# Performance work log

Measured on AMD Instinct MI355X. Metric: run time of the kernel, lower is better.

The kernel has to match this reference:

```python
import jax, jax.numpy as jnp
import numpy as np

B, S, HID = 2, 2048, 1024
NUM_HEADS, HEAD_DIM = 16, 64
GRID_SIZE = 16                 # crop_size // patch_size
ROT_DIM = 2 * (HEAD_DIM // 3 // 2)  # = 20, per axial segment (d, h, w)


def setup_inputs() -> dict:
    key = jax.random.key(0)
    ks = jax.random.split(key, 9)
    sc = 1.0 / np.sqrt(HID)
    return {
        "hidden_states": jax.random.normal(ks[0], (B, S, HID), jnp.float32),
        "Wq": jax.random.normal(ks[1], (HID, HID), jnp.float32) * sc,
        "bq": jax.random.normal(ks[2], (HID,), jnp.float32) * 0.02,
        "Wk": jax.random.normal(ks[3], (HID, HID), jnp.float32) * sc,
        "bk": jax.random.normal(ks[4], (HID,), jnp.float32) * 0.02,
        "Wv": jax.random.normal(ks[5], (HID, HID), jnp.float32) * sc,
        "bv": jax.random.normal(ks[6], (HID,), jnp.float32) * 0.02,
        "Wo": jax.random.normal(ks[7], (HID, HID), jnp.float32) * sc,
        "bo": jax.random.normal(ks[8], (HID,), jnp.float32) * 0.02,
    }


def _rotate(x, pos):
    # x: [B, H, S, D], pos: [S] int. Matches torch rotate_queries_or_keys:
    # sin/cos are TILED (repeat) along the last dim, not interleaved.
    D = x.shape[-1]
    half = D // 2
    omega = 1.0 / (10000.0 ** (jnp.arange(half, dtype=x.dtype) / half))
    freq = pos.astype(x.dtype)[:, None] * omega           # [S, half]
    sin = jnp.tile(jnp.sin(freq), (1, 2))                 # [S, D]
    cos = jnp.tile(jnp.cos(freq), (1, 2))
    y = x.reshape(x.shape[:-1] + (half, 2))
    rot = jnp.stack((-y[..., 1], y[..., 0]), axis=-1).reshape(x.shape)
    return x * cos + rot * sin


def _apply_axial_rope(qk, frame_ids, height_ids, width_ids):
    d = ROT_DIM
    parts = [
        _rotate(qk[..., 0:d], frame_ids),
        _rotate(qk[..., d:2 * d], height_ids),
        _rotate(qk[..., 2 * d:3 * d], width_ids),
    ]
    if 3 * d < qk.shape[-1]:
        parts.append(qk[..., 3 * d:])  # un-rotated tail
    return jnp.concatenate(parts, axis=-1)


def reference(hidden_states, Wq, bq, Wk, bk, Wv, bv, Wo, bo):
    Bq, Sq, _ = hidden_states.shape

    def heads(x):  # [B,S,HID] -> [B,H,S,Dh]
        return x.reshape(Bq, Sq, NUM_HEADS, HEAD_DIM).transpose(0, 2, 1, 3)

    q = heads(hidden_states @ Wq + bq)
    k = heads(hidden_states @ Wk + bk)
    v = heads(hidden_states @ Wv + bv)

    # 3D axial position ids from flat token index
    ids = jnp.arange(Sq)
    tokens_per_frame = GRID_SIZE * GRID_SIZE
    frame_ids = ids // tokens_per_frame
    rem = ids - tokens_per_frame * frame_ids
    height_ids = rem // GRID_SIZE
    width_ids = rem - GRID_SIZE * height_ids

    k = _apply_axial_rope(k, frame_ids, height_ids, width_ids)
    q = _apply_axial_rope(q, frame_ids, height_ids, width_ids)

    scaling = HEAD_DIM ** -0.5
    scores = jnp.einsum("bhqd,bhkd->bhqk", q, k) * scaling
    probs = jax.nn.softmax(scores.astype(jnp.float32), axis=-1).astype(q.dtype)
    ctx = jnp.einsum("bhqk,bhkd->bhqd", probs, v)
    ctx = ctx.transpose(0, 2, 1, 3).reshape(Bq, Sq, HID)
    return ctx @ Wo + bo
```

## Files before the change

kernel.cpp:

```cpp
#include <hip/hip_runtime.h>
#include <hip/hip_bf16.h>

#define B_   2
#define S_   2048
#define HID_ 1024
#define NH_  16
#define HD_  64

typedef __hip_bfloat16 bf16;
typedef __attribute__((ext_vector_type(8))) short s8v;
typedef __attribute__((ext_vector_type(4))) float f4v;

#define QSCALE 0.18033688011112042f

__device__ __forceinline__ unsigned short f2b_rne(float x) {
    unsigned int u = __float_as_uint(x);
    u += 0x7fffu + ((u >> 16) & 1u);
    return (unsigned short)(u >> 16);
}

__device__ __forceinline__ void gload_lds16(const void* g, void* l) {
    __builtin_amdgcn_global_load_lds(
        (const __attribute__((address_space(1))) void*)g,
        (__attribute__((address_space(3))) void*)l, 16, 0, 0);
}

__global__ __launch_bounds__(256) void convert_x_kernel(
    const float* __restrict__ X, unsigned short* __restrict__ Xb)
{
    const int i = (blockIdx.x * 256 + threadIdx.x) * 4;
    const float4 f = *reinterpret_cast<const float4*>(X + i);
    ushort4 u;
    u.x = f2b_rne(f.x); u.y = f2b_rne(f.y); u.z = f2b_rne(f.z); u.w = f2b_rne(f.w);
    *reinterpret_cast<ushort4*>(Xb + i) = u;
}

__global__ __launch_bounds__(256) void transpose_w_kernel(
    const float* __restrict__ W0, const float* __restrict__ W1,
    const float* __restrict__ W2, const float* __restrict__ W3,
    unsigned short* __restrict__ T0, unsigned short* __restrict__ T1,
    unsigned short* __restrict__ T2, unsigned short* __restrict__ T3)
{
    const int z = blockIdx.z;
    const float* __restrict__ W = (z == 0) ? W0 : (z == 1) ? W1 : (z == 2) ? W2 : W3;
    unsigned short* __restrict__ T = (z == 0) ? T0 : (z == 1) ? T1 : (z == 2) ? T2 : T3;

    __shared__ float Tl[64][65];
    const int n0 = blockIdx.x * 64, k0 = blockIdx.y * 64;
    const int t = threadIdx.x;
    const int rr = t >> 4, c4 = (t & 15) * 4;

    #pragma unroll
    for (int i = 0; i < 4; ++i) {
        const int kr = i * 16 + rr;
        const float4 f = *reinterpret_cast<const float4*>(W + (size_t)(k0 + kr) * HID_ + n0 + c4);
        Tl[c4 + 0][kr] = f.x; Tl[c4 + 1][kr] = f.y;
        Tl[c4 + 2][kr] = f.z; Tl[c4 + 3][kr] = f.w;
    }
    __syncthreads();
    #pragma unroll
    for (int i = 0; i < 4; ++i) {
        const int nr = i * 16 + rr;
        ushort4 u;
        u.x = f2b_rne(Tl[nr][c4 + 0]); u.y = f2b_rne(Tl[nr][c4 + 1]);
        u.z = f2b_rne(Tl[nr][c4 + 2]); u.w = f2b_rne(Tl[nr][c4 + 3]);
        *reinterpret_cast<ushort4*>(T + (size_t)(n0 + nr) * HID_ + k0 + c4) = u;
    }
}

__device__ __forceinline__ void mfma_mainloop(
    const unsigned short* __restrict__ Ag, const unsigned short* __restrict__ Bg,
    unsigned short* As, unsigned short* Bs,
    int m0, int n0, int t, f4v acc[4][4])
{
    const int w = t >> 6, lane = t & 63;
    const int l15 = lane & 15, qd = lane >> 4;
    const int wm = (w & 1) * 64, wn = (w >> 1) * 64;
    const int srow = w * 8 + (lane >> 3);
    const int lc8  = (((lane & 7) ^ (lane >> 3)) * 8);

    for (int k0 = 0; k0 < HID_; k0 += 64) {
        __syncthreads();
        #pragma unroll
        for (int it = 0; it < 4; ++it) {
            const int row = it * 32 + srow;
            const int sb = (it * 256 + w * 64) * 8;
            gload_lds16(Ag + (size_t)(m0 + row) * HID_ + k0 + lc8, As + sb);
            gload_lds16(Bg + (size_t)(n0 + row) * HID_ + k0 + lc8, Bs + sb);
        }
        __syncthreads();
        #pragma unroll
        for (int kc = 0; kc < 2; ++kc) {
            const int p = ((kc * 4 + qd) ^ (l15 & 7)) * 8;
            s8v af[4], bf[4];
            #pragma unroll
            for (int mt = 0; mt < 4; ++mt)
                af[mt] = *reinterpret_cast<const s8v*>(As + (wm + mt * 16 + l15) * 64 + p);
            #pragma unroll
            for (int nt = 0; nt < 4; ++nt)
                bf[nt] = *reinterpret_cast<const s8v*>(Bs + (wn + nt * 16 + l15) * 64 + p);
            #pragma unroll
            for (int mt = 0; mt < 4; ++mt)
                #pragma unroll
                for (int nt = 0; nt < 4; ++nt)
                    acc[mt][nt] = __builtin_amdgcn_mfma_f32_16x16x32_bf16(
                        af[mt], bf[nt], acc[mt][nt], 0, 0, 0);
        }
    }
}

__global__ __launch_bounds__(256) void gemm_qkv_kernel(
    const unsigned short* __restrict__ Xb,
    const unsigned short* __restrict__ Wqt, const unsigned short* __restrict__ Wkt,
    const unsigned short* __restrict__ Wvt,
    const float* __restrict__ bq, const float* __restrict__ bk, const float* __restrict__ bv,
    unsigned short* __restrict__ Qb, unsigned short* __restrict__ Kb,
    unsigned short* __restrict__ Vt)
{
    const int z = blockIdx.z;
    const unsigned short* __restrict__ Bt = (z == 0) ? Wqt : (z == 1) ? Wkt : Wvt;
    const float* __restrict__ bias = (z == 0) ? bq : (z == 1) ? bk : bv;

    const int n0 = blockIdx.x * 128, m0 = blockIdx.y * 128;
    const int t = threadIdx.x;
    const int w = t >> 6, lane = t & 63;
    const int l15 = lane & 15, qd = lane >> 4;
    const int wm = (w & 1) * 64, wn = (w >> 1) * 64;

    __shared__ unsigned short As[128 * 64];
    __shared__ unsigned short Bs[128 * 64];

    f4v acc[4][4];
    #pragma unroll
    for (int mt = 0; mt < 4; ++mt)
        #pragma unroll
        for (int nt = 0; nt < 4; ++nt) acc[mt][nt] = (f4v){0.f, 0.f, 0.f, 0.f};

    mfma_mainloop(Xb, Bt, As, Bs, m0, n0, t, acc);

    const float osc = (z == 0) ? QSCALE : 1.f;

    #pragma unroll
    for (int nt = 0; nt < 4; ++nt) {
        const int col = n0 + wn + nt * 16 + l15;
        const int h = col >> 6, d = col & 63;
        const float bsc = bias[col];
        const int seg = d / 20;
        const int ds  = d - seg * 20;
        const float om   = __expf(-0.9210340372f * (float)(ds % 10));
        const float sign = (d & 1) ? 1.f : -1.f;

        #pragma unroll
        for (int mt = 0; mt < 4; ++mt) {
            const int mbase = m0 + wm + mt * 16 + qd * 4;
            const int b = mbase >> 11;
            const int sbase = mbase & 2047;
            if (z == 2) {
                ushort4 u;
                unsigned short* up = (unsigned short*)&u;
                #pragma unroll
                for (int r = 0; r < 4; ++r) up[r] = f2b_rne(acc[mt][nt][r] + bsc);
                *reinterpret_cast<ushort4*>(
                    Vt + ((size_t)(b * NH_ + h) * HD_ + d) * S_ + sbase) = u;
            } else {
                unsigned short* __restrict__ dst = (z == 0 ? Qb : Kb)
                    + ((size_t)(b * NH_ + h) * S_ + sbase) * HD_ + d;
                #pragma unroll
                for (int r = 0; r < 4; ++r) {
                    const int s = sbase + r;
                    float v = acc[mt][nt][r] + bsc;
                    const float xp = __shfl_xor(v, 1);
                    if (d < 60) {
                        const int rem = s & 255;
                        const float pos = (float)(seg == 0 ? (s >> 8)
                                               : (seg == 1 ? (rem >> 4) : (rem & 15)));
                        const float a = pos * om;
                        float sn, cs;
                        __sincosf(a, &sn, &cs);
                        v = v * cs + sign * xp * sn;
                    }
                    dst[(size_t)r * HD_] = f2b_rne(v * osc);
                }
            }
        }
    }
}

__global__ __launch_bounds__(256) void gemm_out_kernel(
    const unsigned short* __restrict__ Cb, const unsigned short* __restrict__ Wot,
    const float* __restrict__ bo, float* __restrict__ out)
{
    const int n0 = blockIdx.x * 128, m0 = blockIdx.y * 128;
    const int t = threadIdx.x;
    const int w = t >> 6, lane = t & 63;
    const int l15 = lane & 15, qd = lane >> 4;
    const int wm = (w & 1) * 64, wn = (w >> 1) * 64;

    __shared__ unsigned short As[128 * 64];
    __shared__ unsigned short Bs[128 * 64];

    f4v acc[4][4];
    #pragma unroll
    for (int mt = 0; mt < 4; ++mt)
        #pragma unroll
        for (int nt = 0; nt < 4; ++nt) acc[mt][nt] = (f4v){0.f, 0.f, 0.f, 0.f};

    mfma_mainloop(Cb, Wot, As, Bs, m0, n0, t, acc);

    #pragma unroll
    for (int nt = 0; nt < 4; ++nt) {
        const int col = n0 + wn + nt * 16 + l15;
        const float bsc = bo[col];
        #pragma unroll
        for (int mt = 0; mt < 4; ++mt) {
            const int mbase = m0 + wm + mt * 16 + qd * 4;
            #pragma unroll
            for (int r = 0; r < 4; ++r)
                out[(size_t)(mbase + r) * HID_ + col] = acc[mt][nt][r] + bsc;
        }
    }
}

__global__ __launch_bounds__(256, 2) void attn_kernel(
    const bf16* __restrict__ Qb, const bf16* __restrict__ Kb,
    const bf16* __restrict__ Vt, unsigned short* __restrict__ CTX)
{
    const int q0 = blockIdx.x * 128;
    const int bh = blockIdx.y;
    const int b  = bh >> 4, h = bh & 15;
    const int t  = threadIdx.x;
    const int w  = t >> 6;
    const int lane = t & 63;
    const int l15 = lane & 15, qd = lane >> 4;

    __shared__ unsigned short Ks[128 * 64];
    __shared__ unsigned short Vs[64 * 128];
    __shared__ unsigned short Ps[128 * 136];

    s8v bq[2][2];
    #pragma unroll
    for (int g = 0; g < 2; ++g) {
        const bf16* Qrow = Qb + ((size_t)bh * S_ + q0 + w * 32 + g * 16 + l15) * HD_ + qd * 8;
        bq[g][0] = *reinterpret_cast<const s8v*>(Qrow);
        bq[g][1] = *reinterpret_cast<const s8v*>(Qrow + 32);
    }

    f4v oacc[2][4];
    float lacc[2] = {0.f, 0.f};
    #pragma unroll
    for (int g = 0; g < 2; ++g)
        #pragma unroll
        for (int dt = 0; dt < 4; ++dt) oacc[g][dt] = (f4v){0.f, 0.f, 0.f, 0.f};

    const bf16* __restrict__ Kg = Kb + (size_t)bh * S_ * HD_;
    const bf16* __restrict__ Vg = Vt + (size_t)bh * HD_ * S_;

    const int krow = lane >> 3;
    const int ksw  = ((lane & 7) ^ krow) * 8;
    const int vrow = lane >> 4;

    for (int k0 = 0; k0 < S_; k0 += 128) {
        __syncthreads();
        #pragma unroll
        for (int it = 0; it < 4; ++it) {
            gload_lds16(Kg + (size_t)(k0 + w * 32 + it * 8 + krow) * HD_ + ksw,
                        Ks + (w * 32 + it * 8) * 64);
        }
        #pragma unroll
        for (int it = 0; it < 4; ++it) {
            const int r = w * 16 + it * 4 + vrow;
            const int sv = ((lane & 15) ^ (r & 15)) * 8;
            gload_lds16(Vg + (size_t)r * S_ + k0 + sv,
                        Vs + (w * 16 + it * 4) * 128);
        }
        __syncthreads();

        #pragma unroll
        for (int nt = 0; nt < 8; ++nt) {
            const unsigned short* kr = Ks + (nt * 16 + l15) * 64;
            const s8v ak0 = *reinterpret_cast<const s8v*>(kr + ((qd ^ (l15 & 7)) * 8));
            const s8v ak1 = *reinterpret_cast<const s8v*>(kr + (((qd + 4) ^ (l15 & 7)) * 8));
            #pragma unroll
            for (int g = 0; g < 2; ++g) {
                f4v zz = (f4v){0.f, 0.f, 0.f, 0.f};
                zz = __builtin_amdgcn_mfma_f32_16x16x32_bf16(ak0, bq[g][0], zz, 0, 0, 0);
                zz = __builtin_amdgcn_mfma_f32_16x16x32_bf16(ak1, bq[g][1], zz, 0, 0, 0);
                const float p0 = __builtin_amdgcn_exp2f(zz[0]);
                const float p1 = __builtin_amdgcn_exp2f(zz[1]);
                const float p2 = __builtin_amdgcn_exp2f(zz[2]);
                const float p3 = __builtin_amdgcn_exp2f(zz[3]);
                const unsigned int u01 = __builtin_amdgcn_perm(
                    __float_as_uint(p1), __float_as_uint(p0), 0x07060302u);
                const unsigned int u23 = __builtin_amdgcn_perm(
                    __float_as_uint(p3), __float_as_uint(p2), 0x07060302u);
                const float t0 = __uint_as_float(u01 << 16);
                const float t1 = __uint_as_float(u01 & 0xffff0000u);
                const float t2 = __uint_as_float(u23 << 16);
                const float t3 = __uint_as_float(u23 & 0xffff0000u);
                lacc[g] += (t0 + t1) + (t2 + t3);
                *reinterpret_cast<uint2*>(
                    Ps + (w * 32 + g * 16 + l15) * 136 + nt * 16 + qd * 4) =
                    make_uint2(u01, u23);
            }
        }

        #pragma unroll
        for (int kc = 0; kc < 4; ++kc) {
            s8v ap[2];
            #pragma unroll
            for (int g = 0; g < 2; ++g)
                ap[g] = *reinterpret_cast<const s8v*>(
                    Ps + (w * 32 + g * 16 + l15) * 136 + kc * 32 + qd * 8);
            #pragma unroll
            for (int dt = 0; dt < 4; ++dt) {
                const s8v bv = *reinterpret_cast<const s8v*>(
                    Vs + (dt * 16 + l15) * 128 + (((kc * 4 + qd) ^ l15) & 15) * 8);
                oacc[0][dt] = __builtin_amdgcn_mfma_f32_16x16x32_bf16(ap[0], bv, oacc[0][dt], 0, 0, 0);
                oacc[1][dt] = __builtin_amdgcn_mfma_f32_16x16x32_bf16(ap[1], bv, oacc[1][dt], 0, 0, 0);
            }
        }
    }

    #pragma unroll
    for (int g = 0; g < 2; ++g) {
        float ls = lacc[g];
        ls += __shfl_xor(ls, 16);
        ls += __shfl_xor(ls, 32);
        #pragma unroll
        for (int r = 0; r < 4; ++r) {
            const float lr = __shfl(ls, qd * 4 + r);
            const float inv = 1.0f / lr;
            const int s = q0 + w * 32 + g * 16 + qd * 4 + r;
            unsigned short* __restrict__ dst =
                CTX + ((size_t)(b * S_ + s)) * HID_ + h * HD_ + l15;
            #pragma unroll
            for (int dt = 0; dt < 4; ++dt)
                dst[dt * 16] = f2b_rne(oacc[g][dt][r] * inv);
        }
    }
}

extern "C" void kernel_launch(void* const* d_in, const int* in_sizes, int n_in,
                              void* d_out, int out_size, void* d_ws, size_t ws_size,
                              hipStream_t stream)
{
    const float* X  = (const float*)d_in[0];
    const float* Wq = (const float*)d_in[1];
    const float* bq = (const float*)d_in[2];
    const float* Wk = (const float*)d_in[3];
    const float* bk = (const float*)d_in[4];
    const float* Wv = (const float*)d_in[5];
    const float* bv = (const float*)d_in[6];
    const float* Wo = (const float*)d_in[7];
    const float* bo = (const float*)d_in[8];
    float* out = (float*)d_out;

    const size_t QKV = (size_t)B_ * NH_ * S_ * HD_;
    unsigned short* Xb  = (unsigned short*)d_ws;
    unsigned short* Wqt = Xb  + QKV;
    unsigned short* Wkt = Wqt + (size_t)HID_ * HID_;
    unsigned short* Wvt = Wkt + (size_t)HID_ * HID_;
    unsigned short* Wot = Wvt + (size_t)HID_ * HID_;
    unsigned short* Qb  = Wot + (size_t)HID_ * HID_;
    unsigned short* Kb  = Qb + QKV;
    unsigned short* Vt  = Kb + QKV;
    unsigned short* Cb  = Vt + QKV;

    convert_x_kernel<<<4096, 256, 0, stream>>>(X, Xb);
    transpose_w_kernel<<<dim3(16, 16, 4), 256, 0, stream>>>(
        Wq, Wk, Wv, Wo, Wqt, Wkt, Wvt, Wot);
    gemm_qkv_kernel<<<dim3(8, 32, 3), 256, 0, stream>>>(
        Xb, Wqt, Wkt, Wvt, bq, bk, bv, Qb, Kb, Vt);
    attn_kernel<<<dim3(S_ / 128, B_ * NH_), 256, 0, stream>>>(
        (const bf16*)Qb, (const bf16*)Kb, (const bf16*)Vt, Cb);
    gemm_out_kernel<<<dim3(8, 32), 256, 0, stream>>>(Cb, Wot, bo, out);
}
```

Before: 208.3 us.

## Keep P in registers for PV MFMA, double-buffer K/V, fuse prep kernels

The attention kernel now feeds the exponentiated scores straight from registers into 16x16x16 bf16 MFMAs against V, dropping the LDS round trip for the P tile. The row sum is computed with an extra MFMA against a ones vector instead of shuffles. K/V tiles are double-buffered with async global-to-LDS loads so the next tile loads while the current one computes. The X conversion and weight transposes are merged into one prep launch. The costs are twice as many smaller MFMAs, more 8-byte V reads from LDS, and twice the LDS for K/V buffers.

```diff
diff --git a/kernel.cpp b/kernel.cpp
--- a/kernel.cpp
+++ b/kernel.cpp
@@ -9,6 +9,7 @@
 
 typedef __hip_bfloat16 bf16;
 typedef __attribute__((ext_vector_type(8))) short s8v;
+typedef __attribute__((ext_vector_type(4))) short s4v;
 typedef __attribute__((ext_vector_type(4))) float f4v;
 
 #define QSCALE 0.18033688011112042f
@@ -25,29 +26,42 @@
         (__attribute__((address_space(3))) void*)l, 16, 0, 0);
 }
 
-__global__ __launch_bounds__(256) void convert_x_kernel(
-    const float* __restrict__ X, unsigned short* __restrict__ Xb)
-{
-    const int i = (blockIdx.x * 256 + threadIdx.x) * 4;
-    const float4 f = *reinterpret_cast<const float4*>(X + i);
-    ushort4 u;
-    u.x = f2b_rne(f.x); u.y = f2b_rne(f.y); u.z = f2b_rne(f.z); u.w = f2b_rne(f.w);
-    *reinterpret_cast<ushort4*>(Xb + i) = u;
-}
-
-__global__ __launch_bounds__(256) void transpose_w_kernel(
+__device__ __forceinline__ s4v pack_p(float p0, float p1, float p2, float p3) {
+    union { uint2 u; s4v s; } c;
+    c.u.x = __builtin_amdgcn_perm(__float_as_uint(p1), __float_as_uint(p0), 0x07060302u);
+    c.u.y = __builtin_amdgcn_perm(__float_as_uint(p3), __float_as_uint(p2), 0x07060302u);
+    return c.s;
+}
+
+__global__ __launch_bounds__(256) void prep_kernel(
+    const float* __restrict__ X,
     const float* __restrict__ W0, const float* __restrict__ W1,
     const float* __restrict__ W2, const float* __restrict__ W3,
+    unsigned short* __restrict__ Xb,
     unsigned short* __restrict__ T0, unsigned short* __restrict__ T1,
     unsigned short* __restrict__ T2, unsigned short* __restrict__ T3)
 {
     const int z = blockIdx.z;
+    const int t = threadIdx.x;
+
+    if (z >= 4) {
+        const size_t base = ((size_t)(z - 4) * 256 + blockIdx.y * 16 + blockIdx.x) * 4096;
+        #pragma unroll
+        for (int p = 0; p < 4; ++p) {
+            const size_t i = base + p * 1024 + t * 4;
+            const float4 f = *reinterpret_cast<const float4*>(X + i);
+            ushort4 u;
+            u.x = f2b_rne(f.x); u.y = f2b_rne(f.y); u.z = f2b_rne(f.z); u.w = f2b_rne(f.w);
+            *reinterpret_cast<ushort4*>(Xb + i) = u;
+        }
+        return;
+    }
+
     const float* __restrict__ W = (z == 0) ? W0 : (z == 1) ? W1 : (z == 2) ? W2 : W3;
     unsigned short* __restrict__ T = (z == 0) ? T0 : (z == 1) ? T1 : (z == 2) ? T2 : T3;
 
     __shared__ float Tl[64][65];
     const int n0 = blockIdx.x * 64, k0 = blockIdx.y * 64;
-    const int t = threadIdx.x;
     const int rr = t >> 4, c4 = (t & 15) * 4;
 
     #pragma unroll
@@ -223,7 +237,7 @@
 
 __global__ __launch_bounds__(256, 2) void attn_kernel(
     const bf16* __restrict__ Qb, const bf16* __restrict__ Kb,
-    const bf16* __restrict__ Vt, unsigned short* __restrict__ CTX)
+    const bf16* __restrict__ Vt, unsigned short* __restrict__ Cb)
 {
     const int q0 = blockIdx.x * 128;
     const int bh = blockIdx.y;
@@ -233,9 +247,8 @@
     const int lane = t & 63;
     const int l15 = lane & 15, qd = lane >> 4;
 
-    __shared__ unsigned short Ks[128 * 64];
-    __shared__ unsigned short Vs[64 * 128];
-    __shared__ unsigned short Ps[128 * 136];
+    __shared__ unsigned short Ks[2][128 * 64];
+    __shared__ unsigned short Vs[2][64 * 128];
 
     s8v bq[2][2];
     #pragma unroll
@@ -246,11 +259,16 @@
     }
 
     f4v oacc[2][4];
-    float lacc[2] = {0.f, 0.f};
-    #pragma unroll
-    for (int g = 0; g < 2; ++g)
+    f4v lones[2];
+    #pragma unroll
+    for (int g = 0; g < 2; ++g) {
+        lones[g] = (f4v){0.f, 0.f, 0.f, 0.f};
         #pragma unroll
         for (int dt = 0; dt < 4; ++dt) oacc[g][dt] = (f4v){0.f, 0.f, 0.f, 0.f};
+    }
+
+    s4v vone;
+    { union { uint2 u; s4v s; } c; c.u = make_uint2(0x3F803F80u, 0x3F803F80u); vone = c.s; }
 
     const bf16* __restrict__ Kg = Kb + (size_t)bh * S_ * HD_;
     const bf16* __restrict__ Vg = Vt + (size_t)bh * HD_ * S_;
@@ -259,27 +277,48 @@
     const int ksw  = ((lane & 7) ^ krow) * 8;
     const int vrow = lane >> 4;
 
-    for (int k0 = 0; k0 < S_; k0 += 128) {
-        __syncthreads();
+    auto stage = [&](int tile, unsigned short* Kd, unsigned short* Vd) {
+        const int k0 = tile * 128;
         #pragma unroll
         for (int it = 0; it < 4; ++it) {
             gload_lds16(Kg + (size_t)(k0 + w * 32 + it * 8 + krow) * HD_ + ksw,
-                        Ks + (w * 32 + it * 8) * 64);
+                        Kd + (w * 32 + it * 8) * 64);
         }
         #pragma unroll
         for (int it = 0; it < 4; ++it) {
             const int r = w * 16 + it * 4 + vrow;
             const int sv = ((lane & 15) ^ (r & 15)) * 8;
             gload_lds16(Vg + (size_t)r * S_ + k0 + sv,
-                        Vs + (w * 16 + it * 4) * 128);
-        }
-        __syncthreads();
+                        Vd + (w * 16 + it * 4) * 128);
+        }
+    };
+
+    stage(0, Ks[0], Vs[0]);
+
+    for (int tt = 0; tt < S_ / 128; ++tt) {
+        __builtin_amdgcn_s_waitcnt(0x0f70);
+        __builtin_amdgcn_s_barrier();
+        if (tt < S_ / 128 - 1)
+            stage(tt + 1, Ks[(tt + 1) & 1], Vs[(tt + 1) & 1]);
+
+        const unsigned short* K_ = Ks[tt & 1];
+        const unsigned short* V_ = Vs[tt & 1];
 
         #pragma unroll
         for (int nt = 0; nt < 8; ++nt) {
-            const unsigned short* kr = Ks + (nt * 16 + l15) * 64;
+            const unsigned short* kr = K_ + (nt * 16 + l15) * 64;
             const s8v ak0 = *reinterpret_cast<const s8v*>(kr + ((qd ^ (l15 & 7)) * 8));
             const s8v ak1 = *reinterpret_cast<const s8v*>(kr + (((qd + 4) ^ (l15 & 7)) * 8));
+
+            s4v bv[4];
+            #pragma unroll
+            for (int dt = 0; dt < 4; ++dt) {
+                const int r = dt * 16 + l15;
+                const int c = nt * 2 + (qd >> 1);
+                bv[dt] = *reinterpret_cast<const s4v*>(
+                    V_ + r * 128 + ((c ^ l15) & 15) * 8 + (qd & 1) * 4);
+            }
+
             #pragma unroll
             for (int g = 0; g < 2; ++g) {
                 f4v zz = (f4v){0.f, 0.f, 0.f, 0.f};
@@ -289,50 +328,25 @@
                 const float p1 = __builtin_amdgcn_exp2f(zz[1]);
                 const float p2 = __builtin_amdgcn_exp2f(zz[2]);
                 const float p3 = __builtin_amdgcn_exp2f(zz[3]);
-                const unsigned int u01 = __builtin_amdgcn_perm(
-                    __float_as_uint(p1), __float_as_uint(p0), 0x07060302u);
-                const unsigned int u23 = __builtin_amdgcn_perm(
-                    __float_as_uint(p3), __float_as_uint(p2), 0x07060302u);
-                const float t0 = __uint_as_float(u01 << 16);
-                const float t1 = __uint_as_float(u01 & 0xffff0000u);
-                const float t2 = __uint_as_float(u23 << 16);
-                const float t3 = __uint_as_float(u23 & 0xffff0000u);
-                lacc[g] += (t0 + t1) + (t2 + t3);
-                *reinterpret_cast<uint2*>(
-                    Ps + (w * 32 + g * 16 + l15) * 136 + nt * 16 + qd * 4) =
-                    make_uint2(u01, u23);
+                const s4v pf = pack_p(p0, p1, p2, p3);
+                #pragma unroll
+                for (int dt = 0; dt < 4; ++dt)
+                    oacc[g][dt] = __builtin_amdgcn_mfma_f32_16x16x16bf16_1k(
+                        pf, bv[dt], oacc[g][dt], 0, 0, 0);
+                lones[g] = __builtin_amdgcn_mfma_f32_16x16x16bf16_1k(
+                    pf, vone, lones[g], 0, 0, 0);
             }
         }
-
-        #pragma unroll
-        for (int kc = 0; kc < 4; ++kc) {
-            s8v ap[2];
-            #pragma unroll
-            for (int g = 0; g < 2; ++g)
-                ap[g] = *reinterpret_cast<const s8v*>(
-                    Ps + (w * 32 + g * 16 + l15) * 136 + kc * 32 + qd * 8);
-            #pragma unroll
-            for (int dt = 0; dt < 4; ++dt) {
-                const s8v bv = *reinterpret_cast<const s8v*>(
-                    Vs + (dt * 16 + l15) * 128 + (((kc * 4 + qd) ^ l15) & 15) * 8);
-                oacc[0][dt] = __builtin_amdgcn_mfma_f32_16x16x32_bf16(ap[0], bv, oacc[0][dt], 0, 0, 0);
-                oacc[1][dt] = __builtin_amdgcn_mfma_f32_16x16x32_bf16(ap[1], bv, oacc[1][dt], 0, 0, 0);
-            }
-        }
     }
 
     #pragma unroll
     for (int g = 0; g < 2; ++g) {
-        float ls = lacc[g];
-        ls += __shfl_xor(ls, 16);
-        ls += __shfl_xor(ls, 32);
         #pragma unroll
         for (int r = 0; r < 4; ++r) {
-            const float lr = __shfl(ls, qd * 4 + r);
-            const float inv = 1.0f / lr;
+            const float inv = 1.0f / lones[g][r];
             const int s = q0 + w * 32 + g * 16 + qd * 4 + r;
             unsigned short* __restrict__ dst =
-                CTX + ((size_t)(b * S_ + s)) * HID_ + h * HD_ + l15;
+                Cb + ((size_t)(b * S_ + s)) * HID_ + h * HD_ + l15;
             #pragma unroll
             for (int dt = 0; dt < 4; ++dt)
                 dst[dt * 16] = f2b_rne(oacc[g][dt][r] * inv);
@@ -356,19 +370,19 @@
     float* out = (float*)d_out;
 
     const size_t QKV = (size_t)B_ * NH_ * S_ * HD_;
-    unsigned short* Xb  = (unsigned short*)d_ws;
+    const size_t WSZ = (size_t)HID_ * HID_;
+    unsigned short* Wot = (unsigned short*)d_ws;
+    unsigned short* Xb  = Wot + WSZ;
     unsigned short* Wqt = Xb  + QKV;
-    unsigned short* Wkt = Wqt + (size_t)HID_ * HID_;
-    unsigned short* Wvt = Wkt + (size_t)HID_ * HID_;
-    unsigned short* Wot = Wvt + (size_t)HID_ * HID_;
-    unsigned short* Qb  = Wot + (size_t)HID_ * HID_;
+    unsigned short* Wkt = Wqt + WSZ;
+    unsigned short* Wvt = Wkt + WSZ;
+    unsigned short* Qb  = Wvt + WSZ;
     unsigned short* Kb  = Qb + QKV;
     unsigned short* Vt  = Kb + QKV;
     unsigned short* Cb  = Vt + QKV;
 
-    convert_x_kernel<<<4096, 256, 0, stream>>>(X, Xb);
-    transpose_w_kernel<<<dim3(16, 16, 4), 256, 0, stream>>>(
-        Wq, Wk, Wv, Wo, Wqt, Wkt, Wvt, Wot);
+    prep_kernel<<<dim3(16, 16, 8), 256, 0, stream>>>(
+        X, Wq, Wk, Wv, Wo, Xb, Wqt, Wkt, Wvt, Wot);
     gemm_qkv_kernel<<<dim3(8, 32, 3), 256, 0, stream>>>(
         Xb, Wqt, Wkt, Wvt, bq, bk, bv, Qb, Kb, Vt);
     attn_kernel<<<dim3(S_ / 128, B_ * NH_), 256, 0, stream>>>(
```

New measurement: 205.9 us. No clear change (-1.2%).
